# Kernel optimization log

Measured on AMD Instinct MI355X. Metric: run time of the kernel, lower is better.

## Reference

```python
import jax, jax.numpy as jnp
import numpy as np

EPS = 1e-12  # F.normalize default eps


def setup_inputs() -> dict:
    key = jax.random.key(0)
    k1, k2, k3, k4 = jax.random.split(key, 4)
    B, N, C, NH = 8, 4096, 512, 8
    x = jax.random.normal(k1, (B, N, C), dtype=jnp.float32)
    Wqkv = jax.random.normal(k2, (3 * C, C), dtype=jnp.float32) * 0.02
    Wproj = jax.random.normal(k3, (C, C), dtype=jnp.float32) * 0.02
    bproj = jax.random.normal(k4, (C,), dtype=jnp.float32) * 0.01
    temp = jnp.ones((NH, 1, 1), dtype=jnp.float32)
    return {"x": x, "Wqkv": Wqkv, "Wproj": Wproj, "bproj": bproj,
            "temp": temp, "H": 64, "W": 64}


def _l2norm(t):
    # normalize along last axis, matching F.normalize(p=2, eps=1e-12)
    return t / jnp.maximum(jnp.linalg.norm(t, axis=-1, keepdims=True), EPS)


def reference(x, Wqkv, Wproj, bproj, temp, H, W):
    B, N, C = x.shape
    nh = temp.shape[0]
    hd = C // nh
    # qkv projection: [B, N, 3, nh, hd]
    qkv = jnp.einsum('bnc,dc->bnd', x, Wqkv).reshape(B, N, 3, nh, hd)
    q = qkv[:, :, 0]  # [B, N, nh, hd]
    k = qkv[:, :, 1]
    v = qkv[:, :, 2]
    # transpose to [B, nh, hd, N] and L2-normalize along tokens (N)
    qn = _l2norm(q.transpose(0, 2, 3, 1))
    kn = _l2norm(k.transpose(0, 2, 3, 1))
    vt = v.transpose(0, 2, 3, 1)  # [B, nh, hd, N]
    # channel attention: [B, nh, hd, hd], scaled by learned per-head temp
    attn = jax.nn.softmax(jnp.einsum('bhcn,bhdn->bhcd', qn, kn) * temp, axis=-1)
    # [B, nh, hd, N] -> [B, N, nh, hd] -> [B, N, C]
    out = jnp.einsum('bhcd,bhdn->bhcn', attn, vt).transpose(0, 3, 1, 2).reshape(B, N, C)
    return jnp.einsum('bnc,dc->bnd', out, Wproj) + bproj
```

## Files before the change

kernel.cpp:

```cpp
#include <hip/hip_runtime.h>
#include <stdint.h>

#define DEVI __device__ __forceinline__

typedef __attribute__((ext_vector_type(8))) short bf16x8;
typedef __attribute__((ext_vector_type(4))) float f32x4;
typedef __attribute__((ext_vector_type(4))) unsigned short u16x4;
typedef __attribute__((ext_vector_type(4))) float float4v;

DEVI unsigned short f2bf(float f) {
  unsigned int u = __builtin_bit_cast(unsigned int, f);
  u += 0x7FFFu + ((u >> 16) & 1u);
  return (unsigned short)(u >> 16);
}
DEVI float bf2f(short s) {
  unsigned int u = ((unsigned int)(unsigned short)s) << 16;
  return __builtin_bit_cast(float, u);
}
DEVI void gload16(const unsigned short* g, unsigned short* l) {
  __builtin_amdgcn_global_load_lds(
      (const __attribute__((address_space(1))) unsigned int*)g,
      (__attribute__((address_space(3))) unsigned int*)l, 16, 0, 0);
}

__global__ void cast_both(const float* __restrict__ x,
                          unsigned short* __restrict__ Xbf,
                          unsigned short* __restrict__ xT) {
  __shared__ float tls[64][65];
  const int n0 = blockIdx.x * 64, c0 = blockIdx.y * 64, b = blockIdx.z;
  const int c = threadIdx.x & 63, rb = threadIdx.x >> 6;
#pragma unroll
  for (int rr = 0; rr < 16; ++rr) {
    int r = rb * 16 + rr;
    float v = x[((size_t)b * 4096 + n0 + r) * 512 + c0 + c];
    tls[r][c] = v;
    Xbf[((size_t)b * 4096 + n0 + r) * 512 + c0 + c] = f2bf(v);
  }
  __syncthreads();
#pragma unroll
  for (int rr = 0; rr < 16; ++rr) {
    int j = rb * 16 + rr;
    xT[((size_t)b * 512 + c0 + j) * 4096 + n0 + c] = f2bf(tls[c][j]);
  }
}

__global__ void prep_w(const float* __restrict__ Wqkv,
                       unsigned short* __restrict__ Wqk,
                       unsigned short* __restrict__ WvT) {
  if (blockIdx.x < 256) {
    const float4v* src = (const float4v*)Wqkv;
    u16x4* dst = (u16x4*)Wqk;
    int base = blockIdx.x * 512 + threadIdx.x;
#pragma unroll
    for (int j = 0; j < 2; ++j) {
      int i = base + j * 256;
      float4v f = src[i];
      u16x4 o;
      o.x = f2bf(f.x); o.y = f2bf(f.y); o.z = f2bf(f.z); o.w = f2bf(f.w);
      dst[i] = o;
    }
  } else {
    __shared__ float tls[64][65];
    const int tile = blockIdx.x - 256;
    const int tr = tile >> 3, tc = tile & 7;
    const int c = threadIdx.x & 63, rb = threadIdx.x >> 6;
#pragma unroll
    for (int rr = 0; rr < 16; ++rr) {
      int r = rb * 16 + rr;
      tls[r][c] = Wqkv[(size_t)(1024 + tr * 64 + r) * 512 + tc * 64 + c];
    }
    __syncthreads();
#pragma unroll
    for (int rr = 0; rr < 16; ++rr) {
      int j = rb * 16 + rr;
      WvT[(size_t)(tc * 64 + j) * 512 + tr * 64 + c] = f2bf(tls[c][j]);
    }
  }
}

template <int STRIDE, int KITERS>
DEVI void gemm_mainloop(const unsigned short* gA, const unsigned short* gB,
                        unsigned short* lA, unsigned short* lB,
                        unsigned short* lAp, unsigned short* lBp,
                        int wr, int wc, int fr, int kg, f32x4 acc[4][4]) {
  for (int kk = 0; kk < KITERS * 32; kk += 32) {
    gload16(gA + kk, lAp);
    gload16(gA + kk + (size_t)64 * STRIDE, lAp + 2048);
    gload16(gB + kk, lBp);
    gload16(gB + kk + (size_t)64 * STRIDE, lBp + 2048);
    __syncthreads();
    bf16x8 af[4], bfv[4];
#pragma unroll
    for (int mi = 0; mi < 4; ++mi)
      af[mi] = *(const bf16x8*)&lA[(wr * 64 + mi * 16 + fr) * 32 + kg * 8];
#pragma unroll
    for (int ni = 0; ni < 4; ++ni)
      bfv[ni] = *(const bf16x8*)&lB[(wc * 64 + ni * 16 + fr) * 32 + kg * 8];
#pragma unroll
    for (int mi = 0; mi < 4; ++mi)
#pragma unroll
      for (int ni = 0; ni < 4; ++ni)
        acc[mi][ni] = __builtin_amdgcn_mfma_f32_16x16x32_bf16(
            af[mi], bfv[ni], acc[mi][ni], 0, 0, 0);
    __syncthreads();
  }
}

__launch_bounds__(256)
__global__ void gsyrk(const unsigned short* __restrict__ xT,
                      float* __restrict__ Gpart) {
  __shared__ __align__(16) unsigned short lA[128 * 32];
  __shared__ __align__(16) unsigned short lB[128 * 32];
  const int tid = threadIdx.x, wave = tid >> 6, lane = tid & 63;
  const int wr = wave >> 1, wc = wave & 1, fr = lane & 15, kg = lane >> 4;
  const int tc = blockIdx.x >> 2, td = blockIdx.x & 3;
  const int chunk = blockIdx.y, b = blockIdx.z;
  const unsigned short* xb = xT + (size_t)b * 512 * 4096 + chunk * 1024;
  f32x4 acc[4][4] = {};
  const int sRow = wave * 16 + (lane >> 2);
  const int sK = (lane & 3) * 8;
  const unsigned short* gA = xb + (size_t)(tc * 128 + sRow) * 4096 + sK;
  const unsigned short* gB = xb + (size_t)(td * 128 + sRow) * 4096 + sK;
  gemm_mainloop<4096, 32>(gA, gB, lA, lB, lA + wave * 512, lB + wave * 512,
                          wr, wc, fr, kg, acc);
  float* Gp = Gpart + (size_t)(chunk * 8 + b) * 512 * 512;
#pragma unroll
  for (int mi = 0; mi < 4; ++mi) {
    const int rbase = tc * 128 + wr * 64 + mi * 16 + kg * 4;
#pragma unroll
    for (int ni = 0; ni < 4; ++ni) {
      const int col = td * 128 + wc * 64 + ni * 16 + fr;
      f32x4 v = acc[mi][ni];
#pragma unroll
      for (int r = 0; r < 4; ++r)
        Gp[(size_t)(rbase + r) * 512 + col] = v[r];
    }
  }
}

__global__ void greduce(const float* __restrict__ Gpart,
                        unsigned short* __restrict__ Gbf) {
  const int stride = gridDim.x * blockDim.x;
  const int n4 = 8 * 512 * 512 / 4;
  for (int i = blockIdx.x * blockDim.x + threadIdx.x; i < n4; i += stride) {
    float4v s = ((const float4v*)Gpart)[i];
#pragma unroll
    for (int c = 1; c < 4; ++c) {
      float4v t = ((const float4v*)(Gpart + (size_t)c * 8 * 512 * 512))[i];
      s.x += t.x; s.y += t.y; s.z += t.z; s.w += t.w;
    }
    u16x4 o;
    o.x = f2bf(s.x); o.y = f2bf(s.y); o.z = f2bf(s.z); o.w = f2bf(s.w);
    ((u16x4*)Gbf)[i] = o;
  }
}

__launch_bounds__(256)
__global__ void tall_gemm(const unsigned short* __restrict__ Wqk,
                          const unsigned short* __restrict__ Gbf,
                          unsigned short* __restrict__ Tbf,
                          float* __restrict__ ssPart) {
  __shared__ __align__(16) unsigned short lA[128 * 32];
  __shared__ __align__(16) unsigned short lB[128 * 32];
  __shared__ float ssL[128][2];
  const int tid = threadIdx.x, wave = tid >> 6, lane = tid & 63;
  const int wr = wave >> 1, wc = wave & 1, fr = lane & 15, kg = lane >> 4;
  const int rowBase = blockIdx.x * 128, colBase = blockIdx.y * 128;
  const int b = blockIdx.z;
  const unsigned short* Gb = Gbf + (size_t)b * 512 * 512;
  f32x4 acc[4][4] = {};
  const int sRow = wave * 16 + (lane >> 2);
  const int sK = (lane & 3) * 8;
  gemm_mainloop<512, 16>(Wqk + (size_t)(rowBase + sRow) * 512 + sK,
                         Gb + (size_t)(colBase + sRow) * 512 + sK,
                         lA, lB, lA + wave * 512, lB + wave * 512,
                         wr, wc, fr, kg, acc);
  unsigned short* Tb = Tbf + (size_t)b * 1024 * 512;
#pragma unroll
  for (int mi = 0; mi < 4; ++mi) {
    const int rbase = rowBase + wr * 64 + mi * 16 + kg * 4;
    f32x4 sacc = {0.f, 0.f, 0.f, 0.f};
#pragma unroll
    for (int ni = 0; ni < 4; ++ni) {
      const int col = colBase + wc * 64 + ni * 16 + fr;
      f32x4 v = acc[mi][ni];
#pragma unroll
      for (int r = 0; r < 4; ++r) {
        float w = bf2f((short)Wqk[(size_t)(rbase + r) * 512 + col]);
        Tb[(size_t)(rbase + r) * 512 + col] = f2bf(v[r]);
        sacc[r] += v[r] * w;
      }
    }
#pragma unroll
    for (int o = 1; o < 16; o <<= 1) {
#pragma unroll
      for (int r = 0; r < 4; ++r) sacc[r] += __shfl_xor(sacc[r], o);
    }
    if (fr == 0) {
#pragma unroll
      for (int r = 0; r < 4; ++r)
        ssL[wr * 64 + mi * 16 + kg * 4 + r][wc] = sacc[r];
    }
  }
  __syncthreads();
  if (tid < 128)
    ssPart[((size_t)blockIdx.y * 8 + b) * 1024 + rowBase + tid] =
        ssL[tid][0] + ssL[tid][1];
}

__launch_bounds__(256)
__global__ void sgemm(const unsigned short* __restrict__ Tbf,
                      const unsigned short* __restrict__ Wqk,
                      float* __restrict__ Sraw) {
  const int bh = blockIdx.x, b = bh >> 3, h = bh & 7;
  const unsigned short* qbase = Tbf + (size_t)(b * 1024 + h * 64) * 512;
  const unsigned short* kbase = Wqk + (size_t)(512 + h * 64) * 512;
  const int wave = threadIdx.x >> 6, lane = threadIdx.x & 63;
  const int wr = wave >> 1, wc = wave & 1, fr = lane & 15, kg = lane >> 4;
  f32x4 acc[2][2] = {};
  for (int kk = 0; kk < 512; kk += 32) {
    bf16x8 a[2], bb[2];
#pragma unroll
    for (int mi = 0; mi < 2; ++mi)
      a[mi] = *(const bf16x8*)(qbase + (size_t)(wr * 32 + mi * 16 + fr) * 512 + kk + kg * 8);
#pragma unroll
    for (int ni = 0; ni < 2; ++ni)
      bb[ni] = *(const bf16x8*)(kbase + (size_t)(wc * 32 + ni * 16 + fr) * 512 + kk + kg * 8);
#pragma unroll
    for (int mi = 0; mi < 2; ++mi)
#pragma unroll
      for (int ni = 0; ni < 2; ++ni)
        acc[mi][ni] = __builtin_amdgcn_mfma_f32_16x16x32_bf16(a[mi], bb[ni], acc[mi][ni], 0, 0, 0);
  }
  float* Sp = Sraw + (size_t)bh * 4096;
#pragma unroll
  for (int mi = 0; mi < 2; ++mi)
#pragma unroll
    for (int ni = 0; ni < 2; ++ni) {
      f32x4 v = acc[mi][ni];
#pragma unroll
      for (int r = 0; r < 4; ++r)
        Sp[(wr * 32 + mi * 16 + kg * 4 + r) * 64 + wc * 32 + ni * 16 + fr] = v[r];
    }
}

__global__ void softmax_kernel(const float* __restrict__ Sraw,
                               const float* __restrict__ ssPart,
                               const float* __restrict__ temp,
                               float* __restrict__ attnOut) {
  const int bh = blockIdx.x;
  const int b = bh >> 3, h = bh & 7;
  const float tmp = temp[h];
  __shared__ float invq[64], invk[64];
  const int t = threadIdx.x;
  if (t < 128) {
    const int r = (t >> 6) * 512 + h * 64 + (t & 63);
    float s = 0.f;
#pragma unroll
    for (int nt = 0; nt < 4; ++nt) s += ssPart[((size_t)nt * 8 + b) * 1024 + r];
    float inv = 1.f / fmaxf(sqrtf(s), 1e-12f);
    if (t < 64) invq[t] = inv;
    else invk[t - 64] = inv;
  }
  __syncthreads();
  const int c = t >> 2, q4 = t & 3;
  float lg[16];
  float mx = -1e30f;
#pragma unroll
  for (int j = 0; j < 16; ++j) {
    const int d = q4 * 16 + j;
    float s = Sraw[(size_t)bh * 4096 + c * 64 + d];
    lg[j] = s * invq[c] * invk[d] * tmp;
    mx = fmaxf(mx, lg[j]);
  }
  mx = fmaxf(mx, __shfl_xor(mx, 1));
  mx = fmaxf(mx, __shfl_xor(mx, 2));
  float sum = 0.f;
#pragma unroll
  for (int j = 0; j < 16; ++j) {
    lg[j] = __expf(lg[j] - mx);
    sum += lg[j];
  }
  sum += __shfl_xor(sum, 1);
  sum += __shfl_xor(sum, 2);
  const float inv = 1.f / sum;
#pragma unroll
  for (int j = 0; j < 16; ++j)
    attnOut[(size_t)bh * 4096 + c * 64 + q4 * 16 + j] = lg[j] * inv;
}

__global__ void weff_kernel(const float* __restrict__ attn,
                            const float* __restrict__ Wproj,
                            unsigned short* __restrict__ Weff) {
  const int bh = blockIdx.x, eb = blockIdx.y;
  const int b = bh >> 3, h = bh & 7;
  __shared__ float at[64 * 64];
  for (int i = threadIdx.x; i < 4096; i += 256)
    at[i] = attn[(size_t)bh * 4096 + i];
  __syncthreads();
  const int e = eb * 64 + (threadIdx.x >> 2);
  const int dq = threadIdx.x & 3;
  float acc[16] = {};
  const float* wrow = Wproj + (size_t)e * 512 + h * 64;
  for (int c = 0; c < 64; ++c) {
    const float w = wrow[c];
#pragma unroll
    for (int j = 0; j < 16; ++j) acc[j] += w * at[c * 64 + dq * 16 + j];
  }
  unsigned short* outp = Weff + ((size_t)b * 512 + e) * 512 + h * 64 + dq * 16;
#pragma unroll
  for (int j = 0; j < 16; ++j) outp[j] = f2bf(acc[j]);
}

__launch_bounds__(256)
__global__ void wcomb_gemm(const unsigned short* __restrict__ WeffAll,
                           const unsigned short* __restrict__ WvT,
                           unsigned short* __restrict__ WcombAll) {
  __shared__ __align__(16) unsigned short lA[128 * 32];
  __shared__ __align__(16) unsigned short lB[128 * 32];
  const int tid = threadIdx.x, wave = tid >> 6, lane = tid & 63;
  const int wr = wave >> 1, wc = wave & 1, fr = lane & 15, kg = lane >> 4;
  const int b = blockIdx.z;
  const int rowBase = blockIdx.x * 128, colBase = blockIdx.y * 128;
  const unsigned short* A = WeffAll + (size_t)b * 512 * 512;
  f32x4 acc[4][4] = {};
  const int sRow = wave * 16 + (lane >> 2);
  const int sK = (lane & 3) * 8;
  gemm_mainloop<512, 16>(A + (size_t)(rowBase + sRow) * 512 + sK,
                         WvT + (size_t)(colBase + sRow) * 512 + sK,
                         lA, lB, lA + wave * 512, lB + wave * 512,
                         wr, wc, fr, kg, acc);
  unsigned short* Wc = WcombAll + (size_t)b * 512 * 512;
#pragma unroll
  for (int mi = 0; mi < 4; ++mi) {
    const int rbase = rowBase + wr * 64 + mi * 16 + kg * 4;
#pragma unroll
    for (int ni = 0; ni < 4; ++ni) {
      const int col = colBase + wc * 64 + ni * 16 + fr;
      f32x4 v = acc[mi][ni];
#pragma unroll
      for (int r = 0; r < 4; ++r)
        Wc[(size_t)(rbase + r) * 512 + col] = f2bf(v[r]);
    }
  }
}

__launch_bounds__(256)
__global__ void out_gemm(const unsigned short* __restrict__ Xbf,
                         const unsigned short* __restrict__ WcombAll,
                         const float* __restrict__ bias,
                         float* __restrict__ out) {
  __shared__ __align__(16) unsigned short lA[128 * 32];
  __shared__ __align__(16) unsigned short lB[128 * 32];
  const int tid = threadIdx.x, wave = tid >> 6, lane = tid & 63;
  const int wr = wave >> 1, wc = wave & 1, fr = lane & 15, kg = lane >> 4;
  const int b = blockIdx.z;
  const int rowBase = blockIdx.x * 128, colBase = blockIdx.y * 128;
  const unsigned short* A = Xbf + (size_t)b * 4096 * 512;
  const unsigned short* Bw = WcombAll + (size_t)b * 512 * 512;
  f32x4 acc[4][4] = {};
  const int sRow = wave * 16 + (lane >> 2);
  const int sK = (lane & 3) * 8;
  gemm_mainloop<512, 16>(A + (size_t)(rowBase + sRow) * 512 + sK,
                         Bw + (size_t)(colBase + sRow) * 512 + sK,
                         lA, lB, lA + wave * 512, lB + wave * 512,
                         wr, wc, fr, kg, acc);
#pragma unroll
  for (int mi = 0; mi < 4; ++mi) {
    const int rbase = rowBase + wr * 64 + mi * 16 + kg * 4;
#pragma unroll
    for (int ni = 0; ni < 4; ++ni) {
      const int col = colBase + wc * 64 + ni * 16 + fr;
      const float bcol = bias[col];
      f32x4 v = acc[mi][ni];
#pragma unroll
      for (int r = 0; r < 4; ++r)
        out[((size_t)b * 4096 + rbase + r) * 512 + col] = v[r] + bcol;
    }
  }
}

extern "C" void kernel_launch(void* const* d_in, const int* in_sizes, int n_in,
                              void* d_out, int out_size, void* d_ws, size_t ws_size,
                              hipStream_t stream) {
  const float* x = (const float*)d_in[0];
  const float* Wqkv = (const float*)d_in[1];
  const float* Wproj = (const float*)d_in[2];
  const float* bproj = (const float*)d_in[3];
  const float* temp = (const float*)d_in[4];
  float* out = (float*)d_out;

  char* ws = (char*)d_ws;
  unsigned short* Xbf = (unsigned short*)(ws + 0);
  unsigned short* xT = (unsigned short*)(ws + 33554432);
  unsigned short* Wqk = (unsigned short*)(ws + 67108864);
  unsigned short* WvT = (unsigned short*)(ws + 68157440);
  float* Gpart = (float*)(ws + 68681728);
  unsigned short* Gbf = (unsigned short*)(ws + 102236160);
  unsigned short* Tbf = (unsigned short*)(ws + 106430464);
  float* ssPart = (float*)(ws + 114819072);
  float* Sraw = (float*)(ws + 114950144);
  float* attn = (float*)(ws + 115998720);
  unsigned short* Weff = (unsigned short*)(ws + 117047296);
  unsigned short* Wcomb = (unsigned short*)(ws + 121241600);

  cast_both<<<dim3(64, 8, 8), 256, 0, stream>>>(x, Xbf, xT);
  prep_w<<<320, 256, 0, stream>>>(Wqkv, Wqk, WvT);
  gsyrk<<<dim3(16, 4, 8), 256, 0, stream>>>(xT, Gpart);
  greduce<<<1024, 256, 0, stream>>>(Gpart, Gbf);
  tall_gemm<<<dim3(8, 4, 8), 256, 0, stream>>>(Wqk, Gbf, Tbf, ssPart);
  sgemm<<<64, 256, 0, stream>>>(Tbf, Wqk, Sraw);
  softmax_kernel<<<64, 256, 0, stream>>>(Sraw, ssPart, temp, attn);
  weff_kernel<<<dim3(64, 8), 256, 0, stream>>>(attn, Wproj, Weff);
  wcomb_gemm<<<dim3(4, 4, 8), 256, 0, stream>>>(Weff, WvT, Wcomb);
  out_gemm<<<dim3(32, 4, 8), 256, 0, stream>>>(Xbf, Wcomb, bproj, out);
}
```

Before: 148.5 us.

## Double-buffer GEMM mainloop, exploit Gram symmetry, fuse prep and softmax kernels

Replaces the single-buffered GEMM mainloop with a double-buffered version that issues the next k-tile's global-to-LDS loads before computing the current one. This overlaps memory latency with MFMA work. The Gram (SYRK) kernel now computes only the upper-triangular 128x128 tiles (10 of 16) and writes the mirrored transpose. The cast and weight-prep kernels are merged into one launch, and the S-GEMM and softmax kernels are fused so the score matrix stays in shared memory. Costs: doubled LDS per block, which may cut occupancy, and strided transpose stores in the Gram epilogue.

```diff
diff --git a/kernel.cpp b/kernel.cpp
--- a/kernel.cpp
+++ b/kernel.cpp
@@ -23,34 +23,36 @@
       (__attribute__((address_space(3))) unsigned int*)l, 16, 0, 0);
 }
 
-__global__ void cast_both(const float* __restrict__ x,
+__global__ void cast_prep(const float* __restrict__ x,
                           unsigned short* __restrict__ Xbf,
-                          unsigned short* __restrict__ xT) {
+                          unsigned short* __restrict__ xT,
+                          const float* __restrict__ Wqkv,
+                          unsigned short* __restrict__ Wqk,
+                          unsigned short* __restrict__ WvT) {
   __shared__ float tls[64][65];
-  const int n0 = blockIdx.x * 64, c0 = blockIdx.y * 64, b = blockIdx.z;
   const int c = threadIdx.x & 63, rb = threadIdx.x >> 6;
-#pragma unroll
-  for (int rr = 0; rr < 16; ++rr) {
-    int r = rb * 16 + rr;
-    float v = x[((size_t)b * 4096 + n0 + r) * 512 + c0 + c];
-    tls[r][c] = v;
-    Xbf[((size_t)b * 4096 + n0 + r) * 512 + c0 + c] = f2bf(v);
-  }
-  __syncthreads();
-#pragma unroll
-  for (int rr = 0; rr < 16; ++rr) {
-    int j = rb * 16 + rr;
-    xT[((size_t)b * 512 + c0 + j) * 4096 + n0 + c] = f2bf(tls[c][j]);
-  }
-}
-
-__global__ void prep_w(const float* __restrict__ Wqkv,
-                       unsigned short* __restrict__ Wqk,
-                       unsigned short* __restrict__ WvT) {
-  if (blockIdx.x < 256) {
+  if (blockIdx.z < 8) {
+    const int n0 = blockIdx.x * 64, c0 = blockIdx.y * 64, b = blockIdx.z;
+#pragma unroll
+    for (int rr = 0; rr < 16; ++rr) {
+      int r = rb * 16 + rr;
+      float v = x[((size_t)b * 4096 + n0 + r) * 512 + c0 + c];
+      tls[r][c] = v;
+      Xbf[((size_t)b * 4096 + n0 + r) * 512 + c0 + c] = f2bf(v);
+    }
+    __syncthreads();
+#pragma unroll
+    for (int rr = 0; rr < 16; ++rr) {
+      int j = rb * 16 + rr;
+      xT[((size_t)b * 512 + c0 + j) * 4096 + n0 + c] = f2bf(tls[c][j]);
+    }
+    return;
+  }
+  const int id = blockIdx.y * 64 + blockIdx.x;
+  if (id < 256) {
     const float4v* src = (const float4v*)Wqkv;
     u16x4* dst = (u16x4*)Wqk;
-    int base = blockIdx.x * 512 + threadIdx.x;
+    int base = id * 512 + threadIdx.x;
 #pragma unroll
     for (int j = 0; j < 2; ++j) {
       int i = base + j * 256;
@@ -59,11 +61,9 @@
       o.x = f2bf(f.x); o.y = f2bf(f.y); o.z = f2bf(f.z); o.w = f2bf(f.w);
       dst[i] = o;
     }
-  } else {
-    __shared__ float tls[64][65];
-    const int tile = blockIdx.x - 256;
+  } else if (id < 320) {
+    const int tile = id - 256;
     const int tr = tile >> 3, tc = tile & 7;
-    const int c = threadIdx.x & 63, rb = threadIdx.x >> 6;
 #pragma unroll
     for (int rr = 0; rr < 16; ++rr) {
       int r = rb * 16 + rr;
@@ -78,24 +78,29 @@
   }
 }
 
-template <int STRIDE, int KITERS>
-DEVI void gemm_mainloop(const unsigned short* gA, const unsigned short* gB,
-                        unsigned short* lA, unsigned short* lB,
-                        unsigned short* lAp, unsigned short* lBp,
-                        int wr, int wc, int fr, int kg, f32x4 acc[4][4]) {
-  for (int kk = 0; kk < KITERS * 32; kk += 32) {
-    gload16(gA + kk, lAp);
-    gload16(gA + kk + (size_t)64 * STRIDE, lAp + 2048);
-    gload16(gB + kk, lBp);
-    gload16(gB + kk + (size_t)64 * STRIDE, lBp + 2048);
-    __syncthreads();
+template <int KITERS>
+DEVI void gemm_db(const unsigned short* gA, int strideA,
+                  const unsigned short* gB, int strideB,
+                  unsigned short (*lA)[4096], unsigned short (*lB)[4096],
+                  int wave, int wr, int wc, int fr, int kg, f32x4 acc[4][4]) {
+  const int wo = wave * 512;
+#define STAGE_T(buf, kk)                                                    \
+  gload16(gA + (kk) * 32, lA[buf] + wo);                                    \
+  gload16(gA + (kk) * 32 + (size_t)64 * strideA, lA[buf] + wo + 2048);      \
+  gload16(gB + (kk) * 32, lB[buf] + wo);                                    \
+  gload16(gB + (kk) * 32 + (size_t)64 * strideB, lB[buf] + wo + 2048);
+  STAGE_T(0, 0);
+  __syncthreads();
+  int cur = 0;
+  for (int kk = 1; kk <= KITERS; ++kk) {
+    if (kk < KITERS) { STAGE_T(cur ^ 1, kk); }
     bf16x8 af[4], bfv[4];
 #pragma unroll
     for (int mi = 0; mi < 4; ++mi)
-      af[mi] = *(const bf16x8*)&lA[(wr * 64 + mi * 16 + fr) * 32 + kg * 8];
+      af[mi] = *(const bf16x8*)&lA[cur][(wr * 64 + mi * 16 + fr) * 32 + kg * 8];
 #pragma unroll
     for (int ni = 0; ni < 4; ++ni)
-      bfv[ni] = *(const bf16x8*)&lB[(wc * 64 + ni * 16 + fr) * 32 + kg * 8];
+      bfv[ni] = *(const bf16x8*)&lB[cur][(wc * 64 + ni * 16 + fr) * 32 + kg * 8];
 #pragma unroll
     for (int mi = 0; mi < 4; ++mi)
 #pragma unroll
@@ -103,37 +108,42 @@
         acc[mi][ni] = __builtin_amdgcn_mfma_f32_16x16x32_bf16(
             af[mi], bfv[ni], acc[mi][ni], 0, 0, 0);
     __syncthreads();
-  }
+    cur ^= 1;
+  }
+#undef STAGE_T
 }
 
 __launch_bounds__(256)
 __global__ void gsyrk(const unsigned short* __restrict__ xT,
                       float* __restrict__ Gpart) {
-  __shared__ __align__(16) unsigned short lA[128 * 32];
-  __shared__ __align__(16) unsigned short lB[128 * 32];
+  __shared__ __align__(16) unsigned short lA[2][4096];
+  __shared__ __align__(16) unsigned short lB[2][4096];
+  static const int PTC[10] = {0, 0, 0, 0, 1, 1, 1, 2, 2, 3};
+  static const int PTD[10] = {0, 1, 2, 3, 1, 2, 3, 2, 3, 3};
   const int tid = threadIdx.x, wave = tid >> 6, lane = tid & 63;
   const int wr = wave >> 1, wc = wave & 1, fr = lane & 15, kg = lane >> 4;
-  const int tc = blockIdx.x >> 2, td = blockIdx.x & 3;
+  const int tc = PTC[blockIdx.x], td = PTD[blockIdx.x];
   const int chunk = blockIdx.y, b = blockIdx.z;
   const unsigned short* xb = xT + (size_t)b * 512 * 4096 + chunk * 1024;
   f32x4 acc[4][4] = {};
   const int sRow = wave * 16 + (lane >> 2);
   const int sK = (lane & 3) * 8;
-  const unsigned short* gA = xb + (size_t)(tc * 128 + sRow) * 4096 + sK;
-  const unsigned short* gB = xb + (size_t)(td * 128 + sRow) * 4096 + sK;
-  gemm_mainloop<4096, 32>(gA, gB, lA, lB, lA + wave * 512, lB + wave * 512,
-                          wr, wc, fr, kg, acc);
+  gemm_db<32>(xb + (size_t)(tc * 128 + sRow) * 4096 + sK, 4096,
+              xb + (size_t)(td * 128 + sRow) * 4096 + sK, 4096,
+              lA, lB, wave, wr, wc, fr, kg, acc);
   float* Gp = Gpart + (size_t)(chunk * 8 + b) * 512 * 512;
 #pragma unroll
   for (int mi = 0; mi < 4; ++mi) {
-    const int rbase = tc * 128 + wr * 64 + mi * 16 + kg * 4;
+    const int rIT = wr * 64 + mi * 16 + kg * 4;
 #pragma unroll
     for (int ni = 0; ni < 4; ++ni) {
-      const int col = td * 128 + wc * 64 + ni * 16 + fr;
+      const int cIT = wc * 64 + ni * 16 + fr;
       f32x4 v = acc[mi][ni];
 #pragma unroll
       for (int r = 0; r < 4; ++r)
-        Gp[(size_t)(rbase + r) * 512 + col] = v[r];
+        Gp[(size_t)(tc * 128 + rIT + r) * 512 + td * 128 + cIT] = v[r];
+      if (tc != td)
+        *(f32x4*)&Gp[(size_t)(td * 128 + cIT) * 512 + tc * 128 + rIT] = v;
     }
   }
 }
@@ -160,8 +170,8 @@
                           const unsigned short* __restrict__ Gbf,
                           unsigned short* __restrict__ Tbf,
                           float* __restrict__ ssPart) {
-  __shared__ __align__(16) unsigned short lA[128 * 32];
-  __shared__ __align__(16) unsigned short lB[128 * 32];
+  __shared__ __align__(16) unsigned short lA[2][4096];
+  __shared__ __align__(16) unsigned short lB[2][4096];
   __shared__ float ssL[128][2];
   const int tid = threadIdx.x, wave = tid >> 6, lane = tid & 63;
   const int wr = wave >> 1, wc = wave & 1, fr = lane & 15, kg = lane >> 4;
@@ -171,10 +181,9 @@
   f32x4 acc[4][4] = {};
   const int sRow = wave * 16 + (lane >> 2);
   const int sK = (lane & 3) * 8;
-  gemm_mainloop<512, 16>(Wqk + (size_t)(rowBase + sRow) * 512 + sK,
-                         Gb + (size_t)(colBase + sRow) * 512 + sK,
-                         lA, lB, lA + wave * 512, lB + wave * 512,
-                         wr, wc, fr, kg, acc);
+  gemm_db<16>(Wqk + (size_t)(rowBase + sRow) * 512 + sK, 512,
+              Gb + (size_t)(colBase + sRow) * 512 + sK, 512,
+              lA, lB, wave, wr, wc, fr, kg, acc);
   unsigned short* Tb = Tbf + (size_t)b * 1024 * 512;
 #pragma unroll
   for (int mi = 0; mi < 4; ++mi) {
@@ -208,14 +217,18 @@
         ssL[tid][0] + ssL[tid][1];
 }
 
-__launch_bounds__(256)
-__global__ void sgemm(const unsigned short* __restrict__ Tbf,
-                      const unsigned short* __restrict__ Wqk,
-                      float* __restrict__ Sraw) {
+__global__ void s_softmax(const unsigned short* __restrict__ Tbf,
+                          const unsigned short* __restrict__ Wqk,
+                          const float* __restrict__ ssPart,
+                          const float* __restrict__ temp,
+                          float* __restrict__ attnOut) {
+  __shared__ float Sl[64 * 64];
+  __shared__ float invq[64], invk[64];
   const int bh = blockIdx.x, b = bh >> 3, h = bh & 7;
   const unsigned short* qbase = Tbf + (size_t)(b * 1024 + h * 64) * 512;
   const unsigned short* kbase = Wqk + (size_t)(512 + h * 64) * 512;
-  const int wave = threadIdx.x >> 6, lane = threadIdx.x & 63;
+  const int t = threadIdx.x;
+  const int wave = t >> 6, lane = t & 63;
   const int wr = wave >> 1, wc = wave & 1, fr = lane & 15, kg = lane >> 4;
   f32x4 acc[2][2] = {};
   for (int kk = 0; kk < 512; kk += 32) {
@@ -232,7 +245,6 @@
       for (int ni = 0; ni < 2; ++ni)
         acc[mi][ni] = __builtin_amdgcn_mfma_f32_16x16x32_bf16(a[mi], bb[ni], acc[mi][ni], 0, 0, 0);
   }
-  float* Sp = Sraw + (size_t)bh * 4096;
 #pragma unroll
   for (int mi = 0; mi < 2; ++mi)
 #pragma unroll
@@ -240,19 +252,8 @@
       f32x4 v = acc[mi][ni];
 #pragma unroll
       for (int r = 0; r < 4; ++r)
-        Sp[(wr * 32 + mi * 16 + kg * 4 + r) * 64 + wc * 32 + ni * 16 + fr] = v[r];
-    }
-}
-
-__global__ void softmax_kernel(const float* __restrict__ Sraw,
-                               const float* __restrict__ ssPart,
-                               const float* __restrict__ temp,
-                               float* __restrict__ attnOut) {
-  const int bh = blockIdx.x;
-  const int b = bh >> 3, h = bh & 7;
-  const float tmp = temp[h];
-  __shared__ float invq[64], invk[64];
-  const int t = threadIdx.x;
+        Sl[(wr * 32 + mi * 16 + kg * 4 + r) * 64 + wc * 32 + ni * 16 + fr] = v[r];
+    }
   if (t < 128) {
     const int r = (t >> 6) * 512 + h * 64 + (t & 63);
     float s = 0.f;
@@ -263,14 +264,14 @@
     else invk[t - 64] = inv;
   }
   __syncthreads();
+  const float tmp = temp[h];
   const int c = t >> 2, q4 = t & 3;
   float lg[16];
   float mx = -1e30f;
 #pragma unroll
   for (int j = 0; j < 16; ++j) {
     const int d = q4 * 16 + j;
-    float s = Sraw[(size_t)bh * 4096 + c * 64 + d];
-    lg[j] = s * invq[c] * invk[d] * tmp;
+    lg[j] = Sl[c * 64 + d] * invq[c] * invk[d] * tmp;
     mx = fmaxf(mx, lg[j]);
   }
   mx = fmaxf(mx, __shfl_xor(mx, 1));
@@ -316,8 +317,8 @@
 __global__ void wcomb_gemm(const unsigned short* __restrict__ WeffAll,
                            const unsigned short* __restrict__ WvT,
                            unsigned short* __restrict__ WcombAll) {
-  __shared__ __align__(16) unsigned short lA[128 * 32];
-  __shared__ __align__(16) unsigned short lB[128 * 32];
+  __shared__ __align__(16) unsigned short lA[2][4096];
+  __shared__ __align__(16) unsigned short lB[2][4096];
   const int tid = threadIdx.x, wave = tid >> 6, lane = tid & 63;
   const int wr = wave >> 1, wc = wave & 1, fr = lane & 15, kg = lane >> 4;
   const int b = blockIdx.z;
@@ -326,10 +327,9 @@
   f32x4 acc[4][4] = {};
   const int sRow = wave * 16 + (lane >> 2);
   const int sK = (lane & 3) * 8;
-  gemm_mainloop<512, 16>(A + (size_t)(rowBase + sRow) * 512 + sK,
-                         WvT + (size_t)(colBase + sRow) * 512 + sK,
-                         lA, lB, lA + wave * 512, lB + wave * 512,
-                         wr, wc, fr, kg, acc);
+  gemm_db<16>(A + (size_t)(rowBase + sRow) * 512 + sK, 512,
+              WvT + (size_t)(colBase + sRow) * 512 + sK, 512,
+              lA, lB, wave, wr, wc, fr, kg, acc);
   unsigned short* Wc = WcombAll + (size_t)b * 512 * 512;
 #pragma unroll
   for (int mi = 0; mi < 4; ++mi) {
@@ -350,8 +350,8 @@
                          const unsigned short* __restrict__ WcombAll,
                          const float* __restrict__ bias,
                          float* __restrict__ out) {
-  __shared__ __align__(16) unsigned short lA[128 * 32];
-  __shared__ __align__(16) unsigned short lB[128 * 32];
+  __shared__ __align__(16) unsigned short lA[2][4096];
+  __shared__ __align__(16) unsigned short lB[2][4096];
   const int tid = threadIdx.x, wave = tid >> 6, lane = tid & 63;
   const int wr = wave >> 1, wc = wave & 1, fr = lane & 15, kg = lane >> 4;
   const int b = blockIdx.z;
@@ -361,10 +361,9 @@
   f32x4 acc[4][4] = {};
   const int sRow = wave * 16 + (lane >> 2);
   const int sK = (lane & 3) * 8;
-  gemm_mainloop<512, 16>(A + (size_t)(rowBase + sRow) * 512 + sK,
-                         Bw + (size_t)(colBase + sRow) * 512 + sK,
-                         lA, lB, lA + wave * 512, lB + wave * 512,
-                         wr, wc, fr, kg, acc);
+  gemm_db<16>(A + (size_t)(rowBase + sRow) * 512 + sK, 512,
+              Bw + (size_t)(colBase + sRow) * 512 + sK, 512,
+              lA, lB, wave, wr, wc, fr, kg, acc);
 #pragma unroll
   for (int mi = 0; mi < 4; ++mi) {
     const int rbase = rowBase + wr * 64 + mi * 16 + kg * 4;
@@ -399,18 +398,15 @@
   unsigned short* Gbf = (unsigned short*)(ws + 102236160);
   unsigned short* Tbf = (unsigned short*)(ws + 106430464);
   float* ssPart = (float*)(ws + 114819072);
-  float* Sraw = (float*)(ws + 114950144);
-  float* attn = (float*)(ws + 115998720);
-  unsigned short* Weff = (unsigned short*)(ws + 117047296);
-  unsigned short* Wcomb = (unsigned short*)(ws + 121241600);
-
-  cast_both<<<dim3(64, 8, 8), 256, 0, stream>>>(x, Xbf, xT);
-  prep_w<<<320, 256, 0, stream>>>(Wqkv, Wqk, WvT);
-  gsyrk<<<dim3(16, 4, 8), 256, 0, stream>>>(xT, Gpart);
+  float* attn = (float*)(ws + 114950144);
+  unsigned short* Weff = (unsigned short*)(ws + 115998720);
+  unsigned short* Wcomb = (unsigned short*)(ws + 120193024);
+
+  cast_prep<<<dim3(64, 8, 9), 256, 0, stream>>>(x, Xbf, xT, Wqkv, Wqk, WvT);
+  gsyrk<<<dim3(10, 4, 8), 256, 0, stream>>>(xT, Gpart);
   greduce<<<1024, 256, 0, stream>>>(Gpart, Gbf);
   tall_gemm<<<dim3(8, 4, 8), 256, 0, stream>>>(Wqk, Gbf, Tbf, ssPart);
-  sgemm<<<64, 256, 0, stream>>>(Tbf, Wqk, Sraw);
-  softmax_kernel<<<64, 256, 0, stream>>>(Sraw, ssPart, temp, attn);
+  s_softmax<<<64, 256, 0, stream>>>(Tbf, Wqk, ssPart, temp, attn);
   weff_kernel<<<dim3(64, 8), 256, 0, stream>>>(attn, Wproj, Weff);
   wcomb_gemm<<<dim3(4, 4, 8), 256, 0, stream>>>(Weff, WvT, Wcomb);
   out_gemm<<<dim3(32, 4, 8), 256, 0, stream>>>(Xbf, Wcomb, bproj, out);
```

Result: faster. 142.3 us (-4.2%).
